# Optimization experiments

Measured on AMD Instinct MI355X. Metric: run time of the kernel, lower is better.

## Reference

```python
import jax, jax.numpy as jnp
import numpy as np

EMBED_DIM = 1024
N_HEADS = 16
HEAD_DIM = EMBED_DIM // N_HEADS
B, T = 4, 2048
LN_EPS = 1e-5


def layernorm(x, gamma, beta):
    mu = jnp.mean(x, axis=-1, keepdims=True)
    var = jnp.var(x, axis=-1, keepdims=True)
    return (x - mu) * jax.lax.rsqrt(var + LN_EPS) * gamma + beta


def setup_inputs() -> dict:
    key = jax.random.key(0)
    ks = jax.random.split(key, 12)
    s = 0.02
    C, H, HD, F = EMBED_DIM, N_HEADS, HEAD_DIM, 4 * EMBED_DIM
    return {
        "x": jax.random.normal(ks[0], (B, T, C), dtype=jnp.float32),
        "Wq": jax.random.normal(ks[1], (H, C, HD), dtype=jnp.float32) * s,
        "Wk": jax.random.normal(ks[2], (H, C, HD), dtype=jnp.float32) * s,
        "Wv": jax.random.normal(ks[3], (H, C, HD), dtype=jnp.float32) * s,
        "Wo": jax.random.normal(ks[4], (C, C), dtype=jnp.float32) * s,
        "bo": jnp.zeros((C,), dtype=jnp.float32),
        "g1": jnp.ones((C,), dtype=jnp.float32),
        "beta1": jnp.zeros((C,), dtype=jnp.float32),
        "g2": jnp.ones((C,), dtype=jnp.float32),
        "beta2": jnp.zeros((C,), dtype=jnp.float32),
        "W1": jax.random.normal(ks[5], (C, F), dtype=jnp.float32) * s,
        "bff1": jnp.zeros((F,), dtype=jnp.float32),
        "W2": jax.random.normal(ks[6], (F, C), dtype=jnp.float32) * s,
        "bff2": jnp.zeros((C,), dtype=jnp.float32),
    }


def reference(x, Wq, Wk, Wv, Wo, bo, g1, beta1, g2, beta2, W1, bff1, W2, bff2):
    Bx, Tx, C = x.shape
    norm_x = layernorm(x, g1, beta1)
    # per-head projections (no bias), stacked: [B, H, T, HD]
    q = jnp.einsum("btc,hcd->bhtd", norm_x, Wq)
    k = jnp.einsum("btc,hcd->bhtd", norm_x, Wk)
    v = jnp.einsum("btc,hcd->bhtd", norm_x, Wv)
    scale = 1.0 / np.sqrt(HEAD_DIM).astype(np.float32)
    scores = jnp.einsum("bhtd,bhsd->bhts", q, k) * scale  # [B,H,T,T]
    causal = jnp.tril(jnp.ones((Tx, Tx), dtype=bool))
    scores = jnp.where(causal, scores, -jnp.inf)
    probs = jax.nn.softmax(scores, axis=-1)
    attn = jnp.einsum("bhts,bhsd->bhtd", probs, v)  # [B,H,T,HD]
    # concat heads -> [B, T, H*HD] then output linear
    attn = jnp.transpose(attn, (0, 2, 1, 3)).reshape(Bx, Tx, C)
    attn_out = attn @ Wo + bo
    res = x + attn_out
    norm_res = layernorm(res, g2, beta2)
    h = jax.nn.gelu(norm_res @ W1 + bff1, approximate=False)
    ffn = h @ W2 + bff2
    return res + ffn
```

## Files before the change

### kernel.cpp

```cpp
#include <hip/hip_runtime.h>
#include <math.h>

constexpr int Bsz = 4, T = 2048, C = 1024, H = 16, HD = 64, F = 4096;
constexpr int M = Bsz * T;
constexpr int NT = T / 64;

typedef _Float16 f16x8 __attribute__((ext_vector_type(8)));
typedef float f32x4 __attribute__((ext_vector_type(4)));
typedef unsigned int u32;

__device__ __forceinline__ void async_copy16(void* lds, const void* g) {
  __builtin_amdgcn_global_load_lds((const __attribute__((address_space(1))) u32*)g,
                                   (__attribute__((address_space(3))) u32*)lds, 16, 0, 0);
}

union H4 { _Float16 h[4]; uint2 u; };

__global__ __launch_bounds__(256) void ln_kernel(const float* __restrict__ x,
                                                 const float* __restrict__ g,
                                                 const float* __restrict__ b,
                                                 _Float16* __restrict__ outh) {
  const int row = blockIdx.x;
  const int tid = threadIdx.x;
  const float4 v = ((const float4*)(x + (size_t)row * C))[tid];
  float s = v.x + v.y + v.z + v.w;
  float ss = v.x * v.x + v.y * v.y + v.z * v.z + v.w * v.w;
#pragma unroll
  for (int off = 32; off > 0; off >>= 1) {
    s += __shfl_xor(s, off, 64);
    ss += __shfl_xor(ss, off, 64);
  }
  __shared__ float red[2][4];
  const int wv = tid >> 6;
  if ((tid & 63) == 0) { red[0][wv] = s; red[1][wv] = ss; }
  __syncthreads();
  s = red[0][0] + red[0][1] + red[0][2] + red[0][3];
  ss = red[1][0] + red[1][1] + red[1][2] + red[1][3];
  const float mu = s * (1.0f / C);
  const float var = ss * (1.0f / C) - mu * mu;
  const float rstd = rsqrtf(var + 1e-5f);
  const float4 gv = ((const float4*)g)[tid];
  const float4 bv = ((const float4*)b)[tid];
  H4 pk;
  pk.h[0] = (_Float16)((v.x - mu) * rstd * gv.x + bv.x);
  pk.h[1] = (_Float16)((v.y - mu) * rstd * gv.y + bv.y);
  pk.h[2] = (_Float16)((v.z - mu) * rstd * gv.z + bv.z);
  pk.h[3] = (_Float16)((v.w - mu) * rstd * gv.w + bv.w);
  ((uint2*)(outh + (size_t)row * C))[tid] = pk.u;
}

__global__ __launch_bounds__(256) void tconv(const float* __restrict__ W,
                                             _Float16* __restrict__ WT,
                                             int K, int N) {
  __shared__ float tile[64][65];
  const int tid = threadIdx.x;
  const int n0 = blockIdx.x * 64, k0 = blockIdx.y * 64;
#pragma unroll
  for (int i = 0; i < 4; ++i) {
    const int idx = i * 1024 + tid * 4;
    const int r = idx >> 6, c = idx & 63;
    const float4 v = *(const float4*)&W[(size_t)(k0 + r) * N + n0 + c];
    tile[r][c] = v.x; tile[r][c + 1] = v.y; tile[r][c + 2] = v.z; tile[r][c + 3] = v.w;
  }
  __syncthreads();
#pragma unroll
  for (int i = 0; i < 4; ++i) {
    const int idx = i * 1024 + tid * 4;
    const int r = idx >> 6, c = idx & 63;
    H4 pk;
#pragma unroll
    for (int j = 0; j < 4; ++j) pk.h[j] = (_Float16)tile[c + j][r];
    *(uint2*)&WT[(size_t)(n0 + r) * K + k0 + c] = pk.u;
  }
}

__global__ __launch_bounds__(256) void tconv_qkv(const float* __restrict__ Wq,
                                                 const float* __restrict__ Wk,
                                                 const float* __restrict__ Wv,
                                                 _Float16* __restrict__ WcatT) {
  __shared__ float tile[64][65];
  const int tid = threadIdx.x;
  const int c0 = blockIdx.x * 64;
  const int h = blockIdx.y, wsel = blockIdx.z;
  const float* W = (wsel == 0 ? Wq : (wsel == 1 ? Wk : Wv)) + (size_t)h * C * HD;
  const int base_row = wsel * 1024 + h * 64;
#pragma unroll
  for (int i = 0; i < 4; ++i) {
    const int idx = i * 1024 + tid * 4;
    const int r = idx >> 6, c = idx & 63;
    const float4 v = *(const float4*)&W[(size_t)(c0 + r) * HD + c];
    tile[r][c] = v.x; tile[r][c + 1] = v.y; tile[r][c + 2] = v.z; tile[r][c + 3] = v.w;
  }
  __syncthreads();
#pragma unroll
  for (int i = 0; i < 4; ++i) {
    const int idx = i * 1024 + tid * 4;
    const int r = idx >> 6, c = idx & 63;
    H4 pk;
#pragma unroll
    for (int j = 0; j < 4; ++j) pk.h[j] = (_Float16)tile[c + j][r];
    *(uint2*)&WcatT[(size_t)(base_row + r) * C + c0 + c] = pk.u;
  }
}

template <int MODE>
__global__ __launch_bounds__(256) void mgemm(const _Float16* __restrict__ Ah,
                                             const _Float16* __restrict__ Bh,
                                             const float* __restrict__ bias,
                                             const float* __restrict__ resid,
                                             float* __restrict__ Of,
                                             _Float16* __restrict__ Oh,
                                             _Float16* __restrict__ Oh2,
                                             _Float16* __restrict__ Oh3,
                                             int Ndim, int Kdim) {
  __shared__ _Float16 Alds[128 * 64];
  __shared__ _Float16 Blds[128 * 64];
  const int tid = threadIdx.x;
  const int wv = tid >> 6, ln = tid & 63;
  const int wm = wv >> 1, wn = wv & 1;
  int bx = blockIdx.x, by = blockIdx.y;
  {
    const int gx = gridDim.x;
    const int nwg = gx * gridDim.y;
    if ((nwg & 7) == 0) {
      int wg = by * gx + bx;
      wg = (wg & 7) * (nwg >> 3) + (wg >> 3);
      bx = wg % gx;
      by = wg / gx;
    }
  }
  const int m0 = by * 128, n0 = bx * 128;
  const int lr = ln & 15, lk = ln >> 4;

  const _Float16* Abase = Ah + (size_t)m0 * Kdim;
  const _Float16* Bbase = Bh + (size_t)n0 * Kdim;

  f32x4 acc[4][4] = {};

  for (int k0 = 0; k0 < Kdim; k0 += 64) {
    __syncthreads();
#pragma unroll
    for (int i = 0; i < 4; ++i) {
      const int seg = wv * 4 + i;
      const int row = seg * 8 + (ln >> 3);
      async_copy16(Alds + seg * 512, Abase + (size_t)row * Kdim + k0 + (ln & 7) * 8);
      async_copy16(Blds + seg * 512, Bbase + (size_t)row * Kdim + k0 + (ln & 7) * 8);
    }
    __syncthreads();
#pragma unroll
    for (int kk = 0; kk < 2; ++kk) {
      f16x8 af[4], bf[4];
#pragma unroll
      for (int fm = 0; fm < 4; ++fm)
        af[fm] = *(const f16x8*)&Alds[(wm * 64 + fm * 16 + lr) * 64 + kk * 32 + lk * 8];
#pragma unroll
      for (int fn = 0; fn < 4; ++fn)
        bf[fn] = *(const f16x8*)&Blds[(wn * 64 + fn * 16 + lr) * 64 + kk * 32 + lk * 8];
      __builtin_amdgcn_s_setprio(1);
#pragma unroll
      for (int fm = 0; fm < 4; ++fm)
#pragma unroll
        for (int fn = 0; fn < 4; ++fn)
          acc[fm][fn] = __builtin_amdgcn_mfma_f32_16x16x32_f16(af[fm], bf[fn], acc[fm][fn], 0, 0, 0);
      __builtin_amdgcn_s_setprio(0);
    }
  }

#pragma unroll
  for (int fm = 0; fm < 4; ++fm) {
#pragma unroll
    for (int fn = 0; fn < 4; ++fn) {
      const int row0 = m0 + wm * 64 + fm * 16 + lk * 4;
      const int col = n0 + wn * 64 + fn * 16 + lr;
      const f32x4 v = acc[fm][fn];
      if (MODE == 0) {
        const int wsel = col >> 10, h = (col >> 6) & 15, d = col & 63;
#pragma unroll
        for (int r = 0; r < 4; ++r) {
          const int m = row0 + r;
          const int bb = m >> 11, t = m & (T - 1);
          if (wsel == 0)
            Oh[(((size_t)bb * H + h) * T + t) * HD + d] = (_Float16)(v[r] * 0.18033688011112042f);
          else if (wsel == 1)
            Oh2[(((size_t)bb * H + h) * T + t) * HD + d] = (_Float16)v[r];
          else
            Oh3[(((size_t)bb * H + h) * HD + d) * T + t] = (_Float16)v[r];
        }
      } else if (MODE == 1 || MODE == 3) {
        const float bc = bias[col];
#pragma unroll
        for (int r = 0; r < 4; ++r)
          Of[(size_t)(row0 + r) * Ndim + col] =
              v[r] + bc + resid[(size_t)(row0 + r) * Ndim + col];
      } else {
        const float bc = bias[col];
#pragma unroll
        for (int r = 0; r < 4; ++r) {
          float t = v[r] + bc;
          t = 0.5f * t * (1.0f + erff(t * 0.70710678118654752f));
          Oh[(size_t)(row0 + r) * Ndim + col] = (_Float16)t;
        }
      }
    }
  }
}

__device__ __forceinline__ void qkt_tile(const f16x8 (&qf)[2],
                                         const _Float16* __restrict__ Kbuf,
                                         f32x4 (&s)[4], int lr, int lk) {
  __builtin_amdgcn_s_setprio(1);
#pragma unroll
  for (int ct = 0; ct < 4; ++ct) {
    s[ct] = f32x4{0.f, 0.f, 0.f, 0.f};
#pragma unroll
    for (int kk = 0; kk < 2; ++kk) {
      const int row = ct * 16 + lr;
      const int ch = (kk * 4 + lk) ^ (row & 7);
      const f16x8 kf = *(const f16x8*)&Kbuf[row * 64 + ch * 8];
      s[ct] = __builtin_amdgcn_mfma_f32_16x16x32_f16(kf, qf[kk], s[ct], 0, 0, 0);
    }
  }
  __builtin_amdgcn_s_setprio(0);
}

__device__ __forceinline__ void online_sm(const f32x4 (&s)[4], float& m_i, float& l_i,
                                          f32x4 (&acc)[4], _Float16 (&ph)[4][4], int l) {
  float mx = fmaxf(fmaxf(s[0][0], s[0][1]), fmaxf(s[0][2], s[0][3]));
#pragma unroll
  for (int ct = 1; ct < 4; ++ct)
    mx = fmaxf(mx, fmaxf(fmaxf(s[ct][0], s[ct][1]), fmaxf(s[ct][2], s[ct][3])));
  mx = fmaxf(mx, __shfl_xor(mx, 16, 64));
  mx = fmaxf(mx, __shfl_xor(mx, 32, 64));
  float mn = fmaxf(m_i, mx);
  if (__all(mx - m_i <= 8.0f)) {
    mn = m_i;
  } else {
    const float alpha = exp2f(m_i - mn);
    m_i = mn;
    l_i *= alpha;
#pragma unroll
    for (int r = 0; r < 4; ++r) {
      const float a_r = __shfl(alpha, (l & 48) | (((l >> 4) & 3) * 4 + r), 64);
#pragma unroll
      for (int dt = 0; dt < 4; ++dt) acc[dt][r] *= a_r;
    }
  }
  float rs = 0.f;
#pragma unroll
  for (int ct = 0; ct < 4; ++ct)
#pragma unroll
    for (int r = 0; r < 4; ++r) {
      const float p = exp2f(s[ct][r] - mn);
      rs += p;
      ph[ct][r] = (_Float16)p;
    }
  rs += __shfl_xor(rs, 16, 64);
  rs += __shfl_xor(rs, 32, 64);
  l_i += rs;
}

__device__ __forceinline__ void pv_tile(const _Float16 (&ph)[4][4], _Float16* Pb,
                                        const _Float16* __restrict__ Vbuf,
                                        f32x4 (&acc)[4], int w, int lr, int lk) {
  const int qw = w * 16 + lr;
#pragma unroll
  for (int ct = 0; ct < 4; ++ct)
#pragma unroll
    for (int r = 0; r < 4; ++r) {
      const int kv = ct * 16 + lk * 4 + r;
      Pb[qw * 64 + (kv ^ ((qw & 7) * 8))] = ph[ct][r];
    }
  __builtin_amdgcn_s_setprio(1);
#pragma unroll
  for (int kk = 0; kk < 2; ++kk) {
    const int pch = (kk * 4 + lk) ^ (qw & 7);
    const f16x8 pa = *(const f16x8*)&Pb[qw * 64 + pch * 8];
#pragma unroll
    for (int dt = 0; dt < 4; ++dt) {
      const int drow = dt * 16 + lr;
      const int vch = (kk * 4 + lk) ^ (drow & 7);
      const f16x8 vf = *(const f16x8*)&Vbuf[drow * 64 + vch * 8];
      acc[dt] = __builtin_amdgcn_mfma_f32_16x16x32_f16(pa, vf, acc[dt], 0, 0, 0);
    }
  }
  __builtin_amdgcn_s_setprio(0);
}

__global__ __launch_bounds__(256) void attn_mfma(const _Float16* __restrict__ Qh,
                                                 const _Float16* __restrict__ Kh,
                                                 const _Float16* __restrict__ Vth,
                                                 _Float16* __restrict__ O) {
  __shared__ _Float16 Kb[2][64 * 64];
  __shared__ _Float16 Vb[2][64 * 64];
  __shared__ _Float16 Pb[64 * 64];
  const int tid = threadIdx.x;
  const int w = tid >> 6, l = tid & 63;
  const int lr = l & 15, lk = l >> 4;
  const int qlo = blockIdx.x, qhi = (NT - 1) - blockIdx.x;
  const int bh = blockIdx.y;
  const _Float16* Qg = Qh + (size_t)bh * T * HD;
  const _Float16* Kg = Kh + (size_t)bh * T * HD;
  const _Float16* Vg = Vth + (size_t)bh * HD * T;

  f16x8 qfl[2], qfh[2];
#pragma unroll
  for (int kk = 0; kk < 2; ++kk) {
    qfl[kk] = *(const f16x8*)&Qg[(size_t)(qlo * 64 + w * 16 + lr) * HD + kk * 32 + lk * 8];
    qfh[kk] = *(const f16x8*)&Qg[(size_t)(qhi * 64 + w * 16 + lr) * HD + kk * 32 + lk * 8];
  }

  f32x4 accl[4] = {}, acch[4] = {};
  float ml = -INFINITY, ll = 0.f, mh = -INFINITY, lh = 0.f;

  const int srow = l >> 3;
  const int schunk = (l & 7) ^ srow;

  int buf = 0;
#pragma unroll
  for (int i = 0; i < 2; ++i) {
    const int seg = w * 2 + i;
    const int rr = seg * 8 + srow;
    async_copy16(&Kb[0][seg * 512], Kg + (size_t)rr * HD + schunk * 8);
    async_copy16(&Vb[0][seg * 512], Vg + (size_t)rr * T + schunk * 8);
  }

  for (int kt = 0; kt <= qhi; ++kt) {
    __syncthreads();
    if (kt < qhi) {
#pragma unroll
      for (int i = 0; i < 2; ++i) {
        const int seg = w * 2 + i;
        const int rr = seg * 8 + srow;
        async_copy16(&Kb[buf ^ 1][seg * 512],
                     Kg + (size_t)((kt + 1) * 64 + rr) * HD + schunk * 8);
        async_copy16(&Vb[buf ^ 1][seg * 512],
                     Vg + (size_t)rr * T + (kt + 1) * 64 + schunk * 8);
      }
    }
    f32x4 s[4];
    _Float16 ph[4][4];
    qkt_tile(qfh, &Kb[buf][0], s, lr, lk);
    if (kt == qhi) {
#pragma unroll
      for (int ct = 0; ct < 4; ++ct)
#pragma unroll
        for (int r = 0; r < 4; ++r)
          if (ct * 16 + lk * 4 + r > w * 16 + lr) s[ct][r] = -INFINITY;
    }
    online_sm(s, mh, lh, acch, ph, l);
    pv_tile(ph, &Pb[0], &Vb[buf][0], acch, w, lr, lk);
    if (kt <= qlo) {
      qkt_tile(qfl, &Kb[buf][0], s, lr, lk);
      if (kt == qlo) {
#pragma unroll
        for (int ct = 0; ct < 4; ++ct)
#pragma unroll
          for (int r = 0; r < 4; ++r)
            if (ct * 16 + lk * 4 + r > w * 16 + lr) s[ct][r] = -INFINITY;
      }
      online_sm(s, ml, ll, accl, ph, l);
      pv_tile(ph, &Pb[0], &Vb[buf][0], accl, w, lr, lk);
    }
    buf ^= 1;
  }
  const int bb = bh >> 4, h = bh & 15;
#pragma unroll
  for (int r = 0; r < 4; ++r) {
    const float lh_r = __shfl(lh, (l & 48) | (lk * 4 + r), 64);
    const float invh = 1.0f / lh_r;
    const int th = qhi * 64 + w * 16 + lk * 4 + r;
#pragma unroll
    for (int dt = 0; dt < 4; ++dt)
      O[((size_t)bb * T + th) * C + h * 64 + dt * 16 + lr] = (_Float16)(acch[dt][r] * invh);
    const float ll_r = __shfl(ll, (l & 48) | (lk * 4 + r), 64);
    const float invl = 1.0f / ll_r;
    const int tl = qlo * 64 + w * 16 + lk * 4 + r;
#pragma unroll
    for (int dt = 0; dt < 4; ++dt)
      O[((size_t)bb * T + tl) * C + h * 64 + dt * 16 + lr] = (_Float16)(accl[dt][r] * invl);
  }
}

extern "C" void kernel_launch(void* const* d_in, const int* in_sizes, int n_in,
                              void* d_out, int out_size, void* d_ws, size_t ws_size,
                              hipStream_t stream) {
  (void)in_sizes; (void)n_in; (void)out_size; (void)ws_size;
  const float* x   = (const float*)d_in[0];
  const float* Wq  = (const float*)d_in[1];
  const float* Wk  = (const float*)d_in[2];
  const float* Wv  = (const float*)d_in[3];
  const float* Wo  = (const float*)d_in[4];
  const float* bo  = (const float*)d_in[5];
  const float* g1  = (const float*)d_in[6];
  const float* be1 = (const float*)d_in[7];
  const float* g2  = (const float*)d_in[8];
  const float* be2 = (const float*)d_in[9];
  const float* W1  = (const float*)d_in[10];
  const float* b1  = (const float*)d_in[11];
  const float* W2  = (const float*)d_in[12];
  const float* b2  = (const float*)d_in[13];
  float* out = (float*)d_out;

  char* base = (char*)d_ws;
  _Float16* norm_h = (_Float16*)base;
  _Float16* WcatT  = (_Float16*)(base + (16ull << 20));
  _Float16* WoT    = (_Float16*)(base + (22ull << 20));
  _Float16* W1T    = (_Float16*)(base + (24ull << 20));
  _Float16* W2T    = (_Float16*)(base + (32ull << 20));
  _Float16* Qhb    = (_Float16*)(base + (40ull << 20));
  _Float16* Khb    = (_Float16*)(base + (56ull << 20));
  _Float16* Vthb   = (_Float16*)(base + (72ull << 20));
  _Float16* attnCh = (_Float16*)(base + (88ull << 20));
  float* res       = (float*)(base + (104ull << 20));
  _Float16* hbuf   = (_Float16*)(base + (40ull << 20));

  tconv_qkv<<<dim3(16, 16, 3), 256, 0, stream>>>(Wq, Wk, Wv, WcatT);
  tconv<<<dim3(16, 16), 256, 0, stream>>>(Wo, WoT, C, C);
  tconv<<<dim3(64, 16), 256, 0, stream>>>(W1, W1T, C, F);
  tconv<<<dim3(16, 64), 256, 0, stream>>>(W2, W2T, F, C);

  ln_kernel<<<M, 256, 0, stream>>>(x, g1, be1, norm_h);
  mgemm<0><<<dim3(3072 / 128, M / 128), 256, 0, stream>>>(
      norm_h, WcatT, nullptr, nullptr, nullptr, Qhb, Khb, Vthb, 3072, C);
  attn_mfma<<<dim3(NT / 2, Bsz * H), 256, 0, stream>>>(Qhb, Khb, Vthb, attnCh);
  mgemm<1><<<dim3(C / 128, M / 128), 256, 0, stream>>>(
      attnCh, WoT, bo, x, res, nullptr, nullptr, nullptr, C, C);
  ln_kernel<<<M, 256, 0, stream>>>(res, g2, be2, norm_h);
  mgemm<2><<<dim3(F / 128, M / 128), 256, 0, stream>>>(
      norm_h, W1T, b1, nullptr, nullptr, hbuf, nullptr, nullptr, F, C);
  mgemm<3><<<dim3(C / 128, M / 128), 256, 0, stream>>>(
      hbuf, W2T, b2, res, out, nullptr, nullptr, nullptr, C, F);
}
```

Before: 616.0 us.

## Rewrite GEMM as 8-wave 256x128 tile with triple-buffered async LDS pipeline

The GEMM kernel now uses 512 threads (8 waves) on a 256x128 output tile. It triple-buffers the A/B k-slices in LDS, using async global-to-LDS copies issued two steps ahead and interleaved with the MFMA halves, with vmcnt-based waits replacing the double syncthreads. LDS rows are XOR-swizzled to avoid bank conflicts. The aim is to hide global load latency, cut barriers, and halve B reloads per output row. In exchange it uses much more LDS (about 144KB), which limits occupancy, and it drops the grid-size guard in the workgroup remap.

Result: faster. 563.7 us (-8.5%).

```diff
diff --git a/kernel.cpp b/kernel.cpp
--- a/kernel.cpp
+++ b/kernel.cpp
@@ -104,66 +104,116 @@
 }
 
 template <int MODE>
-__global__ __launch_bounds__(256) void mgemm(const _Float16* __restrict__ Ah,
-                                             const _Float16* __restrict__ Bh,
-                                             const float* __restrict__ bias,
-                                             const float* __restrict__ resid,
-                                             float* __restrict__ Of,
-                                             _Float16* __restrict__ Oh,
-                                             _Float16* __restrict__ Oh2,
-                                             _Float16* __restrict__ Oh3,
-                                             int Ndim, int Kdim) {
-  __shared__ _Float16 Alds[128 * 64];
-  __shared__ _Float16 Blds[128 * 64];
+__global__ __launch_bounds__(512) void mgemm8(const _Float16* __restrict__ Ah,
+                                              const _Float16* __restrict__ Bh,
+                                              const float* __restrict__ bias,
+                                              const float* __restrict__ resid,
+                                              float* __restrict__ Of,
+                                              _Float16* __restrict__ Oh,
+                                              _Float16* __restrict__ Oh2,
+                                              _Float16* __restrict__ Oh3,
+                                              int Ndim, int Kdim) {
+  __shared__ __attribute__((aligned(16))) _Float16 Alds[3][256 * 64];
+  __shared__ __attribute__((aligned(16))) _Float16 Blds[3][128 * 64];
   const int tid = threadIdx.x;
-  const int wv = tid >> 6, ln = tid & 63;
-  const int wm = wv >> 1, wn = wv & 1;
+  const int wv = tid >> 6, l = tid & 63;
+  const int wm = wv & 3, wn = wv >> 2;
+  const int lr = l & 15, lk = l >> 4;
+  const int srow = l >> 3;
+  const int schunk = (l & 7) ^ srow;
+
   int bx = blockIdx.x, by = blockIdx.y;
   {
     const int gx = gridDim.x;
     const int nwg = gx * gridDim.y;
-    if ((nwg & 7) == 0) {
-      int wg = by * gx + bx;
-      wg = (wg & 7) * (nwg >> 3) + (wg >> 3);
-      bx = wg % gx;
-      by = wg / gx;
-    }
-  }
-  const int m0 = by * 128, n0 = bx * 128;
-  const int lr = ln & 15, lk = ln >> 4;
-
+    int wg = by * gx + bx;
+    wg = (wg & 7) * (nwg >> 3) + (wg >> 3);
+    bx = wg % gx;
+    by = wg / gx;
+  }
+  const int m0 = by * 256, n0 = bx * 128;
   const _Float16* Abase = Ah + (size_t)m0 * Kdim;
   const _Float16* Bbase = Bh + (size_t)n0 * Kdim;
+  const int ksteps = Kdim >> 6;
 
   f32x4 acc[4][4] = {};
 
-  for (int k0 = 0; k0 < Kdim; k0 += 64) {
-    __syncthreads();
-#pragma unroll
-    for (int i = 0; i < 4; ++i) {
-      const int seg = wv * 4 + i;
-      const int row = seg * 8 + (ln >> 3);
-      async_copy16(Alds + seg * 512, Abase + (size_t)row * Kdim + k0 + (ln & 7) * 8);
-      async_copy16(Blds + seg * 512, Bbase + (size_t)row * Kdim + k0 + (ln & 7) * 8);
-    }
-    __syncthreads();
-#pragma unroll
-    for (int kk = 0; kk < 2; ++kk) {
-      f16x8 af[4], bf[4];
-#pragma unroll
-      for (int fm = 0; fm < 4; ++fm)
-        af[fm] = *(const f16x8*)&Alds[(wm * 64 + fm * 16 + lr) * 64 + kk * 32 + lk * 8];
+  auto stage_grp = [&](int t, int grp) {
+    const size_t kofs = (size_t)t << 6;
+    _Float16* Al = &Alds[t % 3][0];
+    _Float16* Bl = &Blds[t % 3][0];
+    if (grp == 0) {
+#pragma unroll
+      for (int i = 0; i < 3; ++i) {
+        const int seg = wv * 4 + i;
+        async_copy16(Al + seg * 512,
+                     Abase + (size_t)(seg * 8 + srow) * Kdim + kofs + schunk * 8);
+      }
+    } else {
+      {
+        const int seg = wv * 4 + 3;
+        async_copy16(Al + seg * 512,
+                     Abase + (size_t)(seg * 8 + srow) * Kdim + kofs + schunk * 8);
+      }
+#pragma unroll
+      for (int i = 0; i < 2; ++i) {
+        const int seg = wv * 2 + i;
+        async_copy16(Bl + seg * 512,
+                     Bbase + (size_t)(seg * 8 + srow) * Kdim + kofs + schunk * 8);
+      }
+    }
+  };
+
+  stage_grp(0, 0); stage_grp(0, 1);
+  stage_grp(1, 0); stage_grp(1, 1);
+
+  for (int t = 0; t < ksteps; ++t) {
+    if (t + 1 < ksteps)
+      asm volatile("s_waitcnt vmcnt(6)" ::: "memory");
+    else
+      asm volatile("s_waitcnt vmcnt(0)" ::: "memory");
+    __builtin_amdgcn_s_barrier();
+    asm volatile("" ::: "memory");
+    const _Float16* Al = &Alds[t % 3][0];
+    const _Float16* Bl = &Blds[t % 3][0];
+
+    f16x8 af[4], bf[4];
+#pragma unroll
+    for (int fm = 0; fm < 4; ++fm) {
+      const int row = wm * 64 + fm * 16 + lr;
+      af[fm] = *(const f16x8*)&Al[row * 64 + (lk ^ (row & 7)) * 8];
+    }
+#pragma unroll
+    for (int fn = 0; fn < 4; ++fn) {
+      const int row = wn * 64 + fn * 16 + lr;
+      bf[fn] = *(const f16x8*)&Bl[row * 64 + (lk ^ (row & 7)) * 8];
+    }
+    if (t + 2 < ksteps) stage_grp(t + 2, 0);
+    __builtin_amdgcn_s_setprio(1);
+#pragma unroll
+    for (int fm = 0; fm < 4; ++fm)
 #pragma unroll
       for (int fn = 0; fn < 4; ++fn)
-        bf[fn] = *(const f16x8*)&Blds[(wn * 64 + fn * 16 + lr) * 64 + kk * 32 + lk * 8];
-      __builtin_amdgcn_s_setprio(1);
-#pragma unroll
-      for (int fm = 0; fm < 4; ++fm)
-#pragma unroll
-        for (int fn = 0; fn < 4; ++fn)
-          acc[fm][fn] = __builtin_amdgcn_mfma_f32_16x16x32_f16(af[fm], bf[fn], acc[fm][fn], 0, 0, 0);
-      __builtin_amdgcn_s_setprio(0);
-    }
+        acc[fm][fn] = __builtin_amdgcn_mfma_f32_16x16x32_f16(af[fm], bf[fn], acc[fm][fn], 0, 0, 0);
+    __builtin_amdgcn_s_setprio(0);
+#pragma unroll
+    for (int fm = 0; fm < 4; ++fm) {
+      const int row = wm * 64 + fm * 16 + lr;
+      af[fm] = *(const f16x8*)&Al[row * 64 + ((4 + lk) ^ (row & 7)) * 8];
+    }
+#pragma unroll
+    for (int fn = 0; fn < 4; ++fn) {
+      const int row = wn * 64 + fn * 16 + lr;
+      bf[fn] = *(const f16x8*)&Bl[row * 64 + ((4 + lk) ^ (row & 7)) * 8];
+    }
+    if (t + 2 < ksteps) stage_grp(t + 2, 1);
+    __builtin_amdgcn_s_setprio(1);
+#pragma unroll
+    for (int fm = 0; fm < 4; ++fm)
+#pragma unroll
+      for (int fn = 0; fn < 4; ++fn)
+        acc[fm][fn] = __builtin_amdgcn_mfma_f32_16x16x32_f16(af[fm], bf[fn], acc[fm][fn], 0, 0, 0);
+    __builtin_amdgcn_s_setprio(0);
   }
 
 #pragma unroll
@@ -196,9 +246,9 @@
         const float bc = bias[col];
 #pragma unroll
         for (int r = 0; r < 4; ++r) {
-          float t = v[r] + bc;
-          t = 0.5f * t * (1.0f + erff(t * 0.70710678118654752f));
-          Oh[(size_t)(row0 + r) * Ndim + col] = (_Float16)t;
+          float tt = v[r] + bc;
+          tt = 0.5f * tt * (1.0f + erff(tt * 0.70710678118654752f));
+          Oh[(size_t)(row0 + r) * Ndim + col] = (_Float16)tt;
         }
       }
     }
@@ -420,14 +470,14 @@
   tconv<<<dim3(16, 64), 256, 0, stream>>>(W2, W2T, F, C);
 
   ln_kernel<<<M, 256, 0, stream>>>(x, g1, be1, norm_h);
-  mgemm<0><<<dim3(3072 / 128, M / 128), 256, 0, stream>>>(
+  mgemm8<0><<<dim3(3072 / 128, M / 256), 512, 0, stream>>>(
       norm_h, WcatT, nullptr, nullptr, nullptr, Qhb, Khb, Vthb, 3072, C);
   attn_mfma<<<dim3(NT / 2, Bsz * H), 256, 0, stream>>>(Qhb, Khb, Vthb, attnCh);
-  mgemm<1><<<dim3(C / 128, M / 128), 256, 0, stream>>>(
+  mgemm8<1><<<dim3(C / 128, M / 256), 512, 0, stream>>>(
       attnCh, WoT, bo, x, res, nullptr, nullptr, nullptr, C, C);
   ln_kernel<<<M, 256, 0, stream>>>(res, g2, be2, norm_h);
-  mgemm<2><<<dim3(F / 128, M / 128), 256, 0, stream>>>(
+  mgemm8<2><<<dim3(F / 128, M / 256), 512, 0, stream>>>(
       norm_h, W1T, b1, nullptr, nullptr, hbuf, nullptr, nullptr, F, C);
-  mgemm<3><<<dim3(C / 128, M / 128), 256, 0, stream>>>(
+  mgemm8<3><<<dim3(C / 128, M / 256), 512, 0, stream>>>(
       hbuf, W2T, b2, res, out, nullptr, nullptr, nullptr, C, F);
 }
```
